# Kernel optimization log

Hardware: AMD Instinct MI355X
Metric: run time of the kernel (lower is better)

Reference implementation:

```python
import jax, jax.numpy as jnp
import numpy as np

B, S, IN, E, H, NL = 64, 512, 1024, 128, 8, 4
D = E // H  # head dim = 16


def setup_inputs() -> dict:
    key = jax.random.key(0)
    ks = jax.random.split(key, 12)
    rn = lambda k, shape: jax.random.normal(k, shape, jnp.float32) * 0.02
    x = jax.random.normal(ks[0], (B, S, IN), jnp.float32)
    # per-recording valid lengths; recording 0 full-length so no attention key row is all-masked
    lengths = jax.random.randint(ks[1], (B,), 1, S + 1).at[0].set(S)
    key_padding_mask = jnp.arange(S)[None, :] >= lengths[:, None]  # (B,S) True = pad
    return {
        'x': x,
        'key_padding_mask': key_padding_mask,
        'embed_w': rn(ks[2], (IN, E)), 'embed_b': jnp.zeros((E,), jnp.float32),
        'qkv_w': rn(ks[3], (NL, 3, E, E)), 'qkv_b': jnp.zeros((NL, 3, E), jnp.float32),
        'out_w': rn(ks[4], (NL, E, E)), 'out_b': jnp.zeros((NL, E), jnp.float32),
        'ln_g': jnp.ones((NL, E), jnp.float32), 'ln_b': jnp.zeros((NL, E), jnp.float32),
        'ff1_w': rn(ks[5], (NL, E, 4 * E)), 'ff1_b': jnp.zeros((NL, 4 * E), jnp.float32),
        'ff2_w': rn(ks[6], (NL, 4 * E, E)), 'ff2_b': jnp.zeros((NL, E), jnp.float32),
        'fc1_w': rn(ks[7], (E, 32)), 'fc1_b': jnp.zeros((32,), jnp.float32),
        'fc2_w': rn(ks[8], (32, 1)), 'fc2_b': jnp.zeros((1,), jnp.float32),
    }


def _ln(x, g, b):
    m = x.mean(-1, keepdims=True)
    v = x.var(-1, keepdims=True)
    return (x - m) / jnp.sqrt(v + 1e-5) * g + b


def _pos_enc(s, e):
    pos = jnp.arange(s, dtype=jnp.float32)[:, None]
    i = jnp.arange(e)[None, :]
    angle = pos / jnp.power(jnp.float32(10000.0), (2 * (i // 2)).astype(jnp.float32) / e)
    return jnp.where(i % 2 == 0, jnp.sin(angle), jnp.cos(angle))  # (S,E)


def reference(x, key_padding_mask, embed_w, embed_b, qkv_w, qkv_b, out_w, out_b,
              ln_g, ln_b, ff1_w, ff1_b, ff2_w, ff2_b, fc1_w, fc1_b, fc2_w, fc2_b):
    h = x @ embed_w + embed_b  # (B,S,E)
    pe = _pos_enc(S, E)
    scale = 1.0 / jnp.sqrt(jnp.float32(D))
    # module uses batch_first=False MHA on (B,S,E): attention runs across recordings.
    # key_padding_mask.T -> (S,B): masked keys are recordings, per epoch position.
    keymask = key_padding_mask.T[:, None, None, :]  # (S,1,1,B)
    for l in range(NL):
        h = h + pe[None]  # pos enc re-added every block (as in source)
        res = h
        q = (h @ qkv_w[l, 0] + qkv_b[l, 0]).reshape(B, S, H, D)
        k = (h @ qkv_w[l, 1] + qkv_b[l, 1]).reshape(B, S, H, D)
        v = (h @ qkv_w[l, 2] + qkv_b[l, 2]).reshape(B, S, H, D)
        scores = jnp.einsum('ishd,jshd->shij', q, k) * scale  # (S,H,B,B)
        scores = jnp.where(keymask, -jnp.inf, scores)
        attn = jax.nn.softmax(scores, axis=-1)
        o = jnp.einsum('shij,jshd->ishd', attn, v).reshape(B, S, E)
        o = o @ out_w[l] + out_b[l]
        h = _ln(o + res, ln_g[l], ln_b[l])
        res = h
        ffo = jax.nn.relu(h @ ff1_w[l] + ff1_b[l]) @ ff2_w[l] + ff2_b[l]
        h = _ln(ffo + res, ln_g[l], ln_b[l])  # same LN params reused, as in source
    # masked mean pool over epochs (vectorized replacement of the python loop)
    valid = (~key_padding_mask).astype(h.dtype)  # (B,S)
    mean = jnp.einsum('bse,bs->be', h, valid) / valid.sum(axis=1)[:, None]
    out = jax.nn.relu(mean @ fc1_w + fc1_b) @ fc2_w + fc2_b  # (B,1)
    return jax.nn.sigmoid(out)
```

## Files before the change

kernel.cpp:

```cpp
#include <hip/hip_runtime.h>

#define Bb 64
#define Ss 512
#define INn 1024
#define Ee 128
#define Hh 8
#define Dd 16
#define NLl 4

typedef unsigned short u16;
typedef __attribute__((ext_vector_type(8))) short short8;
typedef __attribute__((ext_vector_type(4))) float f32x4;

__device__ __forceinline__ float b2f(unsigned u) { return __uint_as_float(u << 16); }
__device__ __forceinline__ u16 f2b(float f) {
    unsigned u = __float_as_uint(f);
    unsigned r = u + 0x7FFFu + ((u >> 16) & 1u);
    return (u16)(r >> 16);
}
__device__ __forceinline__ uint2 pk4(float4 f) {
    uint2 r;
    r.x = (unsigned)f2b(f.x) | ((unsigned)f2b(f.y) << 16);
    r.y = (unsigned)f2b(f.z) | ((unsigned)f2b(f.w) << 16);
    return r;
}

#define GLOAD_LDS16(g, l) __builtin_amdgcn_global_load_lds( \
    (const __attribute__((address_space(1))) void*)(g),     \
    (__attribute__((address_space(3))) void*)(l), 16, 0, 0)

__global__ __launch_bounds__(256) void prep_kernel(const unsigned char* __restrict__ m,
                                                   int* __restrict__ lengths,
                                                   float* __restrict__ pe,
                                                   const float* __restrict__ ew,
                                                   const float* __restrict__ qw,
                                                   const float* __restrict__ ow,
                                                   const float* __restrict__ f1w,
                                                   const float* __restrict__ f2w,
                                                   u16* __restrict__ we, u16* __restrict__ wq,
                                                   u16* __restrict__ wo, u16* __restrict__ wf1,
                                                   u16* __restrict__ wf2) {
    const int bid = blockIdx.x, tid = threadIdx.x;
    if (bid == 0) {
        __shared__ int lf[3];
        __shared__ int part[256];
        if (tid < 3) lf[tid] = 0;
        __syncthreads();
        int l0 = 0, l1 = 0, l23 = 0;
        for (int i = tid * 128; i < tid * 128 + 128; ++i) {
            if (m[i]) { int md = i & 3; if (md == 0) l0 = 1; else if (md == 1) l1 = 1; else l23 = 1; }
        }
        if (l0) atomicOr(&lf[0], 1);
        if (l1) atomicOr(&lf[1], 1);
        if (l23) atomicOr(&lf[2], 1);
        __syncthreads();
        int enc = lf[1] ? 1 : (lf[2] ? 2 : 0);
        int b = tid >> 2, q = tid & 3, cnt = 0;
        for (int s = q * 128; s < q * 128 + 128; ++s) {
            int idx = b * Ss + s;
            int mm;
            if (enc == 1)      mm = (m[idx] != 0);
            else if (enc == 2) mm = (((const float*)(const void*)m)[idx] != 0.0f);
            else               mm = (((const int*)(const void*)m)[idx] != 0);
            cnt += (mm == 0);
        }
        part[tid] = cnt;
        __syncthreads();
        if (tid < 64)
            lengths[tid] = part[tid * 4] + part[tid * 4 + 1] + part[tid * 4 + 2] + part[tid * 4 + 3];
        return;
    }
    if (bid <= 2) {
        for (int i = tid; i < 32768; i += 256) {
            int idx = (bid - 1) * 32768 + i;
            int s = idx >> 7, e = idx & 127;
            float expo = (float)(2 * (e >> 1)) * (1.0f / 128.0f);
            float freq = powf(10000.0f, -expo);
            float angle = (float)s * freq;
            pe[idx] = (e & 1) ? cosf(angle) : sinf(angle);
        }
        return;
    }
    int tb = bid - 3;
    const float* src; u16* dst; int K, N, tile;
    if (tb < 32)       { src = ew;  dst = we;  K = 1024; N = 128; tile = tb; }
    else if (tb < 80)  { int b = tb - 32;  int mat = b >> 2; src = qw  + (size_t)mat * 16384; dst = wq  + (size_t)mat * 16384; K = 128; N = 128; tile = b & 3; }
    else if (tb < 96)  { int b = tb - 80;  int mat = b >> 2; src = ow  + (size_t)mat * 16384; dst = wo  + (size_t)mat * 16384; K = 128; N = 128; tile = b & 3; }
    else if (tb < 160) { int b = tb - 96;  int mat = b >> 4; src = f1w + (size_t)mat * 65536; dst = wf1 + (size_t)mat * 65536; K = 128; N = 512; tile = b & 15; }
    else               { int b = tb - 160; int mat = b >> 4; src = f2w + (size_t)mat * 65536; dst = wf2 + (size_t)mat * 65536; K = 512; N = 128; tile = b & 15; }
    int ktiles = K >> 6;
    int k0 = (tile % ktiles) * 64, n0 = (tile / ktiles) * 64;
    __shared__ __align__(16) u16 t_s[64 * 68];
    int r = tid >> 2, cq = (tid & 3) * 16;
    const float* sp = src + (size_t)(k0 + r) * N + n0 + cq;
#pragma unroll
    for (int i = 0; i < 4; ++i) {
        float4 f = *(const float4*)(sp + 4 * i);
        *(uint2*)&t_s[r * 68 + cq + 4 * i] = pk4(f);
    }
    __syncthreads();
    u16 tmp[16];
#pragma unroll
    for (int kk = 0; kk < 16; ++kk) tmp[kk] = t_s[(cq + kk) * 68 + r];
    int rowg = n0 + r;
    int x = (rowg & 7) << 3;
    u16* base = dst + (size_t)rowg * K;
    *(uint4*)(base + ((k0 + cq) ^ x))     = ((uint4*)tmp)[0];
    *(uint4*)(base + ((k0 + cq + 8) ^ x)) = ((uint4*)tmp)[1];
}

__global__ __launch_bounds__(256) void embed_gemm(const float* __restrict__ X,
                                                  const u16* __restrict__ Wt,
                                                  const float* __restrict__ bias,
                                                  const float* __restrict__ pe,
                                                  u16* __restrict__ C) {
    __shared__ __align__(16) u16 Af[64 * 68];
    __shared__ __align__(16) u16 Bs[128 * 64];
    const int tid = threadIdx.x;
    const int w = tid >> 6, lane = tid & 63, l16 = lane & 15, lhi = lane >> 4;
    const int row0 = blockIdx.x * 64;
    const int xr = (l16 & 7) << 3;
    f32x4 acc[8];
#pragma unroll
    for (int ni = 0; ni < 8; ++ni) acc[ni] = (f32x4){0.f, 0.f, 0.f, 0.f};

    const int ar = tid >> 2, ak = (tid & 3) * 16;
    const int crow = tid >> 3, cc8 = (tid & 7) * 8;
    const int wave_lds = w * 512;
    const u16* Bbase = Wt + cc8;
    const float* Arow = X + (size_t)(row0 + ar) * 1024 + ak;

    for (int k0 = 0; k0 < 1024; k0 += 64) {
        __syncthreads();
#pragma unroll
        for (int i = 0; i < 4; ++i)
            GLOAD_LDS16(Bbase + (size_t)(i * 32 + crow) * 1024 + k0, &Bs[i * 2048 + wave_lds]);
#pragma unroll
        for (int i = 0; i < 4; ++i) {
            float4 f = *(const float4*)(Arow + k0 + 4 * i);
            *(uint2*)&Af[ar * 68 + ak + 4 * i] = pk4(f);
        }
        __syncthreads();
#pragma unroll
        for (int ks = 0; ks < 2; ++ks) {
            short8 af;
            ((uint2*)&af)[0] = *(const uint2*)&Af[(w * 16 + l16) * 68 + ks * 32 + lhi * 8];
            ((uint2*)&af)[1] = *(const uint2*)&Af[(w * 16 + l16) * 68 + ks * 32 + lhi * 8 + 4];
#pragma unroll
            for (int ni = 0; ni < 8; ++ni) {
                short8 bfr = *(const short8*)&Bs[(ni * 16 + l16) * 64 + ((ks * 32 + lhi * 8) ^ xr)];
                acc[ni] = __builtin_amdgcn_mfma_f32_16x16x32_bf16(af, bfr, acc[ni], 0, 0, 0);
            }
        }
    }
    float biasr[8];
#pragma unroll
    for (int ni = 0; ni < 8; ++ni) biasr[ni] = bias[ni * 16 + l16];
#pragma unroll
    for (int reg = 0; reg < 4; ++reg) {
        int r = row0 + w * 16 + lhi * 4 + reg;
        int s = r & 511;
        int bidx = r >> 9;
        int orow = s * 64 + bidx;
        int xo = (bidx & 7) << 3;
        const float* per = pe + (size_t)s * 128;
        u16* crw = C + (size_t)orow * 128;
#pragma unroll
        for (int ni = 0; ni < 8; ++ni) {
            int c = ni * 16 + l16;
            crw[c ^ xo] = f2b(acc[ni][reg] + biasr[ni] + per[c]);
        }
    }
}

__global__ __launch_bounds__(256) void qkv_gemm(const u16* __restrict__ A,
                                                const u16* __restrict__ Wt,
                                                const float* __restrict__ bias,
                                                u16* __restrict__ Cq,
                                                u16* __restrict__ Ckv) {
    __shared__ __align__(16) u16 As[128 * 128];
    __shared__ __align__(16) u16 Bs[128 * 128];
    const int tid = threadIdx.x, w = tid >> 6, lane = tid & 63;
    const int l16 = lane & 15, lhi = lane >> 4;
    const int row0 = blockIdx.x * 128, col0 = blockIdx.y * 128;
    const int so = w * 512 + lane * 8;
    const int xr = (l16 & 7) << 3;
#pragma unroll
    for (int i = 0; i < 8; ++i) {
        GLOAD_LDS16(A + (size_t)row0 * 128 + i * 2048 + so, &As[i * 2048 + w * 512]);
        GLOAD_LDS16(Wt + (size_t)col0 * 128 + i * 2048 + so, &Bs[i * 2048 + w * 512]);
    }
    __syncthreads();
    f32x4 acc[2][8];
#pragma unroll
    for (int mi = 0; mi < 2; ++mi)
#pragma unroll
        for (int ni = 0; ni < 8; ++ni) acc[mi][ni] = (f32x4){0.f, 0.f, 0.f, 0.f};
#pragma unroll
    for (int ks = 0; ks < 4; ++ks) {
        const int ko = (ks * 32 + lhi * 8) ^ xr;
        short8 af[2], bfr[8];
#pragma unroll
        for (int mi = 0; mi < 2; ++mi)
            af[mi] = *(const short8*)&As[(w * 32 + mi * 16 + l16) * 128 + ko];
#pragma unroll
        for (int ni = 0; ni < 8; ++ni)
            bfr[ni] = *(const short8*)&Bs[(ni * 16 + l16) * 128 + ko];
#pragma unroll
        for (int mi = 0; mi < 2; ++mi)
#pragma unroll
            for (int ni = 0; ni < 8; ++ni)
                acc[mi][ni] = __builtin_amdgcn_mfma_f32_16x16x32_bf16(af[mi], bfr[ni], acc[mi][ni], 0, 0, 0);
    }
    float biasr[8];
#pragma unroll
    for (int ni = 0; ni < 8; ++ni) biasr[ni] = bias[col0 + ni * 16 + l16];
#pragma unroll
    for (int mi = 0; mi < 2; ++mi)
#pragma unroll
        for (int reg = 0; reg < 4; ++reg) {
            int r = row0 + w * 32 + mi * 16 + lhi * 4 + reg;
            u16* crw; int cbase;
            if (col0 == 0) { crw = Cq + (size_t)r * 128; cbase = 0; }
            else           { crw = Ckv + (size_t)r * 256; cbase = col0 - 128; }
#pragma unroll
            for (int ni = 0; ni < 8; ++ni)
                crw[cbase + ni * 16 + l16] = f2b(acc[mi][ni][reg] + biasr[ni]);
        }
}

__global__ __launch_bounds__(256) void attnout_kernel(const u16* __restrict__ qb,
                                                      const u16* __restrict__ kvb,
                                                      const u16* __restrict__ wo,
                                                      const float* __restrict__ outb,
                                                      const int* __restrict__ lengths,
                                                      const float* __restrict__ gamma,
                                                      const float* __restrict__ beta,
                                                      u16* __restrict__ h) {
    const int s = blockIdx.x;
    const int tid = threadIdx.x, w = tid >> 6, lane = tid & 63;
    const int l16 = lane & 15, lhi = lane >> 4;
    __shared__ __align__(16) u16 Vt[8 * 16 * 72];
    __shared__ __align__(16) u16 Ps[4 * 64 * 72];
    __shared__ __align__(16) u16 o_s[64 * 136];
    __shared__ int len_s[64];

    {
        int j = tid >> 2, c = tid & 3;
        const u16* src = kvb + ((size_t)(s * 64 + j)) * 256 + 128 + c * 32;
        u16 tmp[32];
        ((uint4*)tmp)[0] = *(const uint4*)src;
        ((uint4*)tmp)[1] = *(const uint4*)(src + 8);
        ((uint4*)tmp)[2] = *(const uint4*)(src + 16);
        ((uint4*)tmp)[3] = *(const uint4*)(src + 24);
#pragma unroll
        for (int e = 0; e < 32; ++e) {
            int hh = 2 * c + (e >> 4), d = e & 15;
            Vt[hh * 1152 + d * 72 + j] = tmp[e];
        }
    }
    if (tid < 64) len_s[tid] = lengths[tid];
    __syncthreads();

    bool mk[4];
#pragma unroll
    for (int jt = 0; jt < 4; ++jt) mk[jt] = (s >= len_s[jt * 16 + l16]);

    u16* pw = Ps + w * 4608;
#pragma unroll
    for (int hp = 0; hp < 2; ++hp) {
        const int hh = w * 2 + hp;
        short8 af[4];
#pragma unroll
        for (int it = 0; it < 4; ++it) {
            af[it] = (short8){0, 0, 0, 0, 0, 0, 0, 0};
            if (lhi < 2)
                af[it] = *(const short8*)(qb + ((size_t)(s * 64 + it * 16 + l16)) * 128 + hh * 16 + lhi * 8);
        }
        f32x4 sf[4][4];
#pragma unroll
        for (int jt = 0; jt < 4; ++jt) {
            short8 bf = (short8){0, 0, 0, 0, 0, 0, 0, 0};
            if (lhi < 2)
                bf = *(const short8*)(kvb + ((size_t)(s * 64 + jt * 16 + l16)) * 256 + hh * 16 + lhi * 8);
#pragma unroll
            for (int it = 0; it < 4; ++it)
                sf[it][jt] = __builtin_amdgcn_mfma_f32_16x16x32_bf16(af[it], bf, (f32x4){0.f, 0.f, 0.f, 0.f}, 0, 0, 0);
        }
        float inv[4][4];
#pragma unroll
        for (int it = 0; it < 4; ++it) {
#pragma unroll
            for (int reg = 0; reg < 4; ++reg) {
                float vv[4], mx = -1e30f;
#pragma unroll
                for (int jt = 0; jt < 4; ++jt) {
                    float xv = mk[jt] ? -1e30f : sf[it][jt][reg] * 0.25f;
                    vv[jt] = xv; mx = fmaxf(mx, xv);
                }
                mx = fmaxf(mx, __shfl_xor(mx, 1)); mx = fmaxf(mx, __shfl_xor(mx, 2));
                mx = fmaxf(mx, __shfl_xor(mx, 4)); mx = fmaxf(mx, __shfl_xor(mx, 8));
                float e4[4], sum = 0.f;
#pragma unroll
                for (int jt = 0; jt < 4; ++jt) {
                    float e = mk[jt] ? 0.f : __expf(vv[jt] - mx);
                    e4[jt] = e; sum += e;
                }
                sum += __shfl_xor(sum, 1); sum += __shfl_xor(sum, 2);
                sum += __shfl_xor(sum, 4); sum += __shfl_xor(sum, 8);
                inv[it][reg] = 1.0f / sum;
                int prow = it * 16 + lhi * 4 + reg;
#pragma unroll
                for (int jt = 0; jt < 4; ++jt)
                    pw[prow * 72 + jt * 16 + l16] = f2b(e4[jt]);
            }
        }
        f32x4 ao[4];
#pragma unroll
        for (int it = 0; it < 4; ++it) ao[it] = (f32x4){0.f, 0.f, 0.f, 0.f};
        short8 vb[2];
#pragma unroll
        for (int ksv = 0; ksv < 2; ++ksv)
            vb[ksv] = *(const short8*)&Vt[hh * 1152 + l16 * 72 + ksv * 32 + lhi * 8];
#pragma unroll
        for (int it = 0; it < 4; ++it)
#pragma unroll
            for (int ksv = 0; ksv < 2; ++ksv) {
                short8 pa = *(const short8*)&pw[(it * 16 + l16) * 72 + ksv * 32 + lhi * 8];
                ao[it] = __builtin_amdgcn_mfma_f32_16x16x32_bf16(pa, vb[ksv], ao[it], 0, 0, 0);
            }
#pragma unroll
        for (int it = 0; it < 4; ++it)
#pragma unroll
            for (int reg = 0; reg < 4; ++reg)
                o_s[(it * 16 + lhi * 4 + reg) * 136 + hh * 16 + l16] = f2b(ao[it][reg] * inv[it][reg]);
    }
    __syncthreads();

    const int xr = (l16 & 7) << 3;
    f32x4 acc[8];
#pragma unroll
    for (int ni = 0; ni < 8; ++ni) acc[ni] = (f32x4){0.f, 0.f, 0.f, 0.f};
#pragma unroll
    for (int ks = 0; ks < 4; ++ks) {
        short8 af = *(const short8*)&o_s[(w * 16 + l16) * 136 + ks * 32 + lhi * 8];
#pragma unroll
        for (int ni = 0; ni < 8; ++ni) {
            short8 bf = *(const short8*)(wo + (size_t)(ni * 16 + l16) * 128 + ((ks * 32 + lhi * 8) ^ xr));
            acc[ni] = __builtin_amdgcn_mfma_f32_16x16x32_bf16(af, bf, acc[ni], 0, 0, 0);
        }
    }
    float biasr[8], gr[8], br[8];
#pragma unroll
    for (int ni = 0; ni < 8; ++ni) {
        int c = ni * 16 + l16;
        biasr[ni] = outb[c]; gr[ni] = gamma[c]; br[ni] = beta[c];
    }
#pragma unroll
    for (int reg = 0; reg < 4; ++reg) {
        int row = w * 16 + lhi * 4 + reg;
        int xo = (row & 7) << 3;
        size_t rbase = ((size_t)(s * 64 + row)) * 128;
        float v[8], sm = 0.f, s2 = 0.f;
#pragma unroll
        for (int ni = 0; ni < 8; ++ni) {
            float x = acc[ni][reg] + biasr[ni] + b2f(h[rbase + ((ni * 16 + l16) ^ xo)]);
            v[ni] = x; sm += x; s2 += x * x;
        }
        sm += __shfl_xor(sm, 1); sm += __shfl_xor(sm, 2);
        sm += __shfl_xor(sm, 4); sm += __shfl_xor(sm, 8);
        s2 += __shfl_xor(s2, 1); s2 += __shfl_xor(s2, 2);
        s2 += __shfl_xor(s2, 4); s2 += __shfl_xor(s2, 8);
        float mean = sm * (1.0f / 128.0f);
        float var = s2 * (1.0f / 128.0f) - mean * mean;
        float rstd = rsqrtf(fmaxf(var, 0.0f) + 1e-5f);
#pragma unroll
        for (int ni = 0; ni < 8; ++ni)
            h[rbase + ((ni * 16 + l16) ^ xo)] = f2b((v[ni] - mean) * rstd * gr[ni] + br[ni]);
    }
}

__global__ __launch_bounds__(256) void ff_fused(const u16* __restrict__ hbuf,
                                                const u16* __restrict__ w1t,
                                                const u16* __restrict__ w2t,
                                                const float* __restrict__ b1,
                                                const float* __restrict__ b2,
                                                const float* __restrict__ gamma,
                                                const float* __restrict__ beta,
                                                const float* __restrict__ pe,
                                                u16* __restrict__ hout) {
    __shared__ __align__(16) u16 A_s[16384];
    __shared__ __align__(16) u16 W1_s[16384];
    __shared__ __align__(16) u16 W2_s[16384];
    __shared__ __align__(16) u16 T_s[16384];
    const int tid = threadIdx.x, w = tid >> 6, lane = tid & 63;
    const int l16 = lane & 15, lhi = lane >> 4;
    const int row0 = blockIdx.x * 128;
    const int so = w * 512 + lane * 8;
    const int xr = (l16 & 7) << 3;
#pragma unroll
    for (int i = 0; i < 8; ++i)
        GLOAD_LDS16(hbuf + (size_t)row0 * 128 + i * 2048 + so, &A_s[i * 2048 + w * 512]);

    f32x4 acc2[2][8];
#pragma unroll
    for (int mi = 0; mi < 2; ++mi)
#pragma unroll
        for (int ni = 0; ni < 8; ++ni) acc2[mi][ni] = (f32x4){0.f, 0.f, 0.f, 0.f};

    for (int nc = 0; nc < 4; ++nc) {
        __syncthreads();
#pragma unroll
        for (int i = 0; i < 8; ++i) {
            GLOAD_LDS16(w1t + nc * 16384 + i * 2048 + so, &W1_s[i * 2048 + w * 512]);
            int slot = i * 2048 + so;
            GLOAD_LDS16(w2t + (size_t)(slot >> 7) * 512 + nc * 128 + (slot & 127),
                        &W2_s[i * 2048 + w * 512]);
        }
        __syncthreads();
        f32x4 acc1[2][8];
#pragma unroll
        for (int mi = 0; mi < 2; ++mi)
#pragma unroll
            for (int ni = 0; ni < 8; ++ni) acc1[mi][ni] = (f32x4){0.f, 0.f, 0.f, 0.f};
#pragma unroll
        for (int ks = 0; ks < 4; ++ks) {
            const int ko = (ks * 32 + lhi * 8) ^ xr;
            short8 af[2], bfr[8];
#pragma unroll
            for (int mi = 0; mi < 2; ++mi)
                af[mi] = *(const short8*)&A_s[(w * 32 + mi * 16 + l16) * 128 + ko];
#pragma unroll
            for (int ni = 0; ni < 8; ++ni)
                bfr[ni] = *(const short8*)&W1_s[(ni * 16 + l16) * 128 + ko];
#pragma unroll
            for (int mi = 0; mi < 2; ++mi)
#pragma unroll
                for (int ni = 0; ni < 8; ++ni)
                    acc1[mi][ni] = __builtin_amdgcn_mfma_f32_16x16x32_bf16(af[mi], bfr[ni], acc1[mi][ni], 0, 0, 0);
        }
        float bb[8];
#pragma unroll
        for (int ni = 0; ni < 8; ++ni) bb[ni] = b1[nc * 128 + ni * 16 + l16];
#pragma unroll
        for (int mi = 0; mi < 2; ++mi)
#pragma unroll
            for (int reg = 0; reg < 4; ++reg) {
                int xt = ((lhi * 4 + reg) & 7) << 3;
#pragma unroll
                for (int ni = 0; ni < 8; ++ni)
                    T_s[(w * 32 + mi * 16 + lhi * 4 + reg) * 128 + ((ni * 16 + l16) ^ xt)] =
                        f2b(fmaxf(acc1[mi][ni][reg] + bb[ni], 0.0f));
            }
#pragma unroll
        for (int ks = 0; ks < 4; ++ks) {
            const int ko = (ks * 32 + lhi * 8) ^ xr;
            short8 pa[2], bfr[8];
#pragma unroll
            for (int mi = 0; mi < 2; ++mi)
                pa[mi] = *(const short8*)&T_s[(w * 32 + mi * 16 + l16) * 128 + ko];
#pragma unroll
            for (int ni = 0; ni < 8; ++ni)
                bfr[ni] = *(const short8*)&W2_s[(ni * 16 + l16) * 128 + ko];
#pragma unroll
            for (int mi = 0; mi < 2; ++mi)
#pragma unroll
                for (int ni = 0; ni < 8; ++ni)
                    acc2[mi][ni] = __builtin_amdgcn_mfma_f32_16x16x32_bf16(pa[mi], bfr[ni], acc2[mi][ni], 0, 0, 0);
        }
    }
    float b2r[8], gr[8], br[8];
#pragma unroll
    for (int ni = 0; ni < 8; ++ni) {
        int c = ni * 16 + l16;
        b2r[ni] = b2[c]; gr[ni] = gamma[c]; br[ni] = beta[c];
    }
#pragma unroll
    for (int mi = 0; mi < 2; ++mi)
#pragma unroll
        for (int reg = 0; reg < 4; ++reg) {
            int lrow = w * 32 + mi * 16 + lhi * 4 + reg;
            int r = row0 + lrow;
            int xo = (lrow & 7) << 3;
            float v[8], sm = 0.f, s2 = 0.f;
#pragma unroll
            for (int ni = 0; ni < 8; ++ni) {
                float x = acc2[mi][ni][reg] + b2r[ni] + b2f(A_s[lrow * 128 + ((ni * 16 + l16) ^ xo)]);
                v[ni] = x; sm += x; s2 += x * x;
            }
            sm += __shfl_xor(sm, 1); sm += __shfl_xor(sm, 2);
            sm += __shfl_xor(sm, 4); sm += __shfl_xor(sm, 8);
            s2 += __shfl_xor(s2, 1); s2 += __shfl_xor(s2, 2);
            s2 += __shfl_xor(s2, 4); s2 += __shfl_xor(s2, 8);
            float mean = sm * (1.0f / 128.0f);
            float var = s2 * (1.0f / 128.0f) - mean * mean;
            float rstd = rsqrtf(fmaxf(var, 0.0f) + 1e-5f);
            u16* crw = hout + (size_t)r * 128;
#pragma unroll
            for (int ni = 0; ni < 8; ++ni) {
                int c = ni * 16 + l16;
                float val = (v[ni] - mean) * rstd * gr[ni] + br[ni];
                if (pe) val += pe[(size_t)(r >> 6) * 128 + c];
                crw[c ^ xo] = f2b(val);
            }
        }
}

__global__ __launch_bounds__(256) void poolhead_kernel(const u16* __restrict__ h,
                                                       const int* __restrict__ lengths,
                                                       const float* __restrict__ fc1w,
                                                       const float* __restrict__ fc1b,
                                                       const float* __restrict__ fc2w,
                                                       const float* __restrict__ fc2b,
                                                       float* __restrict__ out) {
    int b = blockIdx.x, tid = threadIdx.x;
    int e = tid & 127, half = tid >> 7;
    int len = lengths[b];
    int ep = e ^ ((b & 7) << 3);
    float s = 0.0f;
    for (int t = half; t < len; t += 2) s += b2f(h[((size_t)(t * 64 + b)) * 128 + ep]);
    __shared__ float red[256];
    __shared__ float mp[128];
    __shared__ float z[32];
    red[tid] = s;
    __syncthreads();
    if (tid < 128) mp[tid] = (red[tid] + red[tid + 128]) / (float)len;
    __syncthreads();
    if (tid < 32) {
        float a = fc1b[tid];
        for (int k = 0; k < 128; ++k) a = fmaf(mp[k], fc1w[k * 32 + tid], a);
        z[tid] = fmaxf(a, 0.0f);
    }
    __syncthreads();
    if (tid == 0) {
        float a = fc2b[0];
#pragma unroll
        for (int t = 0; t < 32; ++t) a = fmaf(z[t], fc2w[t], a);
        out[b] = 1.0f / (1.0f + expf(-a));
    }
}

extern "C" void kernel_launch(void* const* d_in, const int* in_sizes, int n_in,
                              void* d_out, int out_size, void* d_ws, size_t ws_size,
                              hipStream_t stream) {
    (void)in_sizes; (void)n_in; (void)out_size; (void)ws_size;
    const float* x        = (const float*)d_in[0];
    const unsigned char* mask = (const unsigned char*)d_in[1];
    const float* embed_w  = (const float*)d_in[2];
    const float* embed_b  = (const float*)d_in[3];
    const float* qkv_w    = (const float*)d_in[4];
    const float* qkv_b    = (const float*)d_in[5];
    const float* out_w    = (const float*)d_in[6];
    const float* out_b    = (const float*)d_in[7];
    const float* ln_g     = (const float*)d_in[8];
    const float* ln_b     = (const float*)d_in[9];
    const float* ff1_w    = (const float*)d_in[10];
    const float* ff1_b    = (const float*)d_in[11];
    const float* ff2_w    = (const float*)d_in[12];
    const float* ff2_b    = (const float*)d_in[13];
    const float* fc1_w    = (const float*)d_in[14];
    const float* fc1_b    = (const float*)d_in[15];
    const float* fc2_w    = (const float*)d_in[16];
    const float* fc2_b    = (const float*)d_in[17];

    char* wsb = (char*)d_ws;
    int*   lengths = (int*)wsb;
    float* pe      = (float*)(wsb + 512);
    u16* wt_embed  = (u16*)(wsb + 262656);
    u16* wt_qkv    = (u16*)(wsb + 524800);
    u16* wt_out    = (u16*)(wsb + 918016);
    u16* wt_ff1    = (u16*)(wsb + 1049088);
    u16* wt_ff2    = (u16*)(wsb + 1573376);
    u16* hbuf      = (u16*)(wsb + 2097664);
    u16* qb        = (u16*)(wsb + 10486272);
    u16* kvb       = (u16*)(wsb + 18874880);

    prep_kernel<<<227, 256, 0, stream>>>(mask, lengths, pe,
                                         embed_w, qkv_w, out_w, ff1_w, ff2_w,
                                         wt_embed, wt_qkv, wt_out, wt_ff1, wt_ff2);

    embed_gemm<<<512, 256, 0, stream>>>(x, wt_embed, embed_b, pe, hbuf);

    for (int l = 0; l < NLl; ++l) {
        qkv_gemm<<<dim3(256, 3), 256, 0, stream>>>(
            hbuf, wt_qkv + (size_t)l * 49152, qkv_b + l * 384, qb, kvb);
        attnout_kernel<<<512, 256, 0, stream>>>(
            qb, kvb, wt_out + (size_t)l * 16384, out_b + l * 128,
            lengths, ln_g + l * 128, ln_b + l * 128, hbuf);
        ff_fused<<<256, 256, 0, stream>>>(
            hbuf, wt_ff1 + (size_t)l * 65536, wt_ff2 + (size_t)l * 65536,
            ff1_b + l * 512, ff2_b + l * 128,
            ln_g + l * 128, ln_b + l * 128, (l < 3) ? pe : nullptr, hbuf);
    }

    poolhead_kernel<<<64, 256, 0, stream>>>(hbuf, lengths, fc1_w, fc1_b, fc2_w, fc2_b,
                                            (float*)d_out);
}
```

Baseline: 427.7 us.

## Fuse next-layer QKV projection into FF kernel and double-buffer weight loads

Folds the next layer's QKV projection into the tail of ff_fused: the LN output tile is kept in shared memory and multiplied by the next layer's QKV weights loaded into the freed LDS arena. This removes three separate qkv_gemm launches and their re-read of hbuf. The FF weight loads are restructured so the next W1/W2 chunks are prefetched while the current chunk computes, and embed_gemm double-buffers its B tile. In exchange, ff_fused uses a 128KB LDS arena, which limits occupancy, and each block does more work in its epilogue.

```diff
diff --git a/kernel.cpp b/kernel.cpp
--- a/kernel.cpp
+++ b/kernel.cpp
@@ -115,7 +115,7 @@
                                                   const float* __restrict__ pe,
                                                   u16* __restrict__ C) {
     __shared__ __align__(16) u16 Af[64 * 68];
-    __shared__ __align__(16) u16 Bs[128 * 64];
+    __shared__ __align__(16) u16 Bs[2][128 * 64];
     const int tid = threadIdx.x;
     const int w = tid >> 6, lane = tid & 63, l16 = lane & 15, lhi = lane >> 4;
     const int row0 = blockIdx.x * 64;
@@ -130,17 +130,25 @@
     const u16* Bbase = Wt + cc8;
     const float* Arow = X + (size_t)(row0 + ar) * 1024 + ak;
 
-    for (int k0 = 0; k0 < 1024; k0 += 64) {
+#pragma unroll
+    for (int i = 0; i < 4; ++i)
+        GLOAD_LDS16(Bbase + (size_t)(i * 32 + crow) * 1024, &Bs[0][i * 2048 + wave_lds]);
+
+    for (int it = 0; it < 16; ++it) {
+        const int k0 = it * 64;
         __syncthreads();
-#pragma unroll
-        for (int i = 0; i < 4; ++i)
-            GLOAD_LDS16(Bbase + (size_t)(i * 32 + crow) * 1024 + k0, &Bs[i * 2048 + wave_lds]);
 #pragma unroll
         for (int i = 0; i < 4; ++i) {
             float4 f = *(const float4*)(Arow + k0 + 4 * i);
             *(uint2*)&Af[ar * 68 + ak + 4 * i] = pk4(f);
         }
         __syncthreads();
+        if (it < 15) {
+#pragma unroll
+            for (int i = 0; i < 4; ++i)
+                GLOAD_LDS16(Bbase + (size_t)(i * 32 + crow) * 1024 + k0 + 64,
+                            &Bs[(it + 1) & 1][i * 2048 + wave_lds]);
+        }
 #pragma unroll
         for (int ks = 0; ks < 2; ++ks) {
             short8 af;
@@ -148,7 +156,7 @@
             ((uint2*)&af)[1] = *(const uint2*)&Af[(w * 16 + l16) * 68 + ks * 32 + lhi * 8 + 4];
 #pragma unroll
             for (int ni = 0; ni < 8; ++ni) {
-                short8 bfr = *(const short8*)&Bs[(ni * 16 + l16) * 64 + ((ks * 32 + lhi * 8) ^ xr)];
+                short8 bfr = *(const short8*)&Bs[it & 1][(ni * 16 + l16) * 64 + ((ks * 32 + lhi * 8) ^ xr)];
                 acc[ni] = __builtin_amdgcn_mfma_f32_16x16x32_bf16(af, bfr, acc[ni], 0, 0, 0);
             }
         }
@@ -388,19 +396,33 @@
                                                 const float* __restrict__ gamma,
                                                 const float* __restrict__ beta,
                                                 const float* __restrict__ pe,
-                                                u16* __restrict__ hout) {
-    __shared__ __align__(16) u16 A_s[16384];
-    __shared__ __align__(16) u16 W1_s[16384];
-    __shared__ __align__(16) u16 W2_s[16384];
-    __shared__ __align__(16) u16 T_s[16384];
+                                                u16* __restrict__ hout,
+                                                const u16* __restrict__ wqn,
+                                                const float* __restrict__ qbn,
+                                                u16* __restrict__ Cq,
+                                                u16* __restrict__ Ckv) {
+    __shared__ __align__(16) u16 arena[65536];
+    u16* A_s  = arena;
+    u16* W1_s = arena + 16384;
+    u16* W2_s = arena + 32768;
+    u16* T_s  = arena + 49152;
+    u16* Wq_s = arena + 16384;
     const int tid = threadIdx.x, w = tid >> 6, lane = tid & 63;
     const int l16 = lane & 15, lhi = lane >> 4;
     const int row0 = blockIdx.x * 128;
     const int so = w * 512 + lane * 8;
     const int xr = (l16 & 7) << 3;
+
 #pragma unroll
     for (int i = 0; i < 8; ++i)
         GLOAD_LDS16(hbuf + (size_t)row0 * 128 + i * 2048 + so, &A_s[i * 2048 + w * 512]);
+#pragma unroll
+    for (int i = 0; i < 8; ++i) {
+        GLOAD_LDS16(w1t + i * 2048 + so, &W1_s[i * 2048 + w * 512]);
+        int slot = i * 2048 + so;
+        GLOAD_LDS16(w2t + (size_t)(slot >> 7) * 512 + (slot & 127), &W2_s[i * 2048 + w * 512]);
+    }
+    __syncthreads();
 
     f32x4 acc2[2][8];
 #pragma unroll
@@ -409,15 +431,6 @@
         for (int ni = 0; ni < 8; ++ni) acc2[mi][ni] = (f32x4){0.f, 0.f, 0.f, 0.f};
 
     for (int nc = 0; nc < 4; ++nc) {
-        __syncthreads();
-#pragma unroll
-        for (int i = 0; i < 8; ++i) {
-            GLOAD_LDS16(w1t + nc * 16384 + i * 2048 + so, &W1_s[i * 2048 + w * 512]);
-            int slot = i * 2048 + so;
-            GLOAD_LDS16(w2t + (size_t)(slot >> 7) * 512 + nc * 128 + (slot & 127),
-                        &W2_s[i * 2048 + w * 512]);
-        }
-        __syncthreads();
         f32x4 acc1[2][8];
 #pragma unroll
         for (int mi = 0; mi < 2; ++mi)
@@ -452,6 +465,12 @@
                     T_s[(w * 32 + mi * 16 + lhi * 4 + reg) * 128 + ((ni * 16 + l16) ^ xt)] =
                         f2b(fmaxf(acc1[mi][ni][reg] + bb[ni], 0.0f));
             }
+        __syncthreads();
+        if (nc < 3) {
+#pragma unroll
+            for (int i = 0; i < 8; ++i)
+                GLOAD_LDS16(w1t + (nc + 1) * 16384 + i * 2048 + so, &W1_s[i * 2048 + w * 512]);
+        }
 #pragma unroll
         for (int ks = 0; ks < 4; ++ks) {
             const int ko = (ks * 32 + lhi * 8) ^ xr;
@@ -468,6 +487,20 @@
                 for (int ni = 0; ni < 8; ++ni)
                     acc2[mi][ni] = __builtin_amdgcn_mfma_f32_16x16x32_bf16(pa[mi], bfr[ni], acc2[mi][ni], 0, 0, 0);
         }
+        __syncthreads();
+        if (nc < 3) {
+#pragma unroll
+            for (int i = 0; i < 8; ++i) {
+                int slot = i * 2048 + so;
+                GLOAD_LDS16(w2t + (size_t)(slot >> 7) * 512 + (nc + 1) * 128 + (slot & 127),
+                            &W2_s[i * 2048 + w * 512]);
+            }
+        }
+    }
+    if (wqn) {
+#pragma unroll
+        for (int i = 0; i < 24; ++i)
+            GLOAD_LDS16(wqn + i * 2048 + so, &Wq_s[i * 2048 + w * 512]);
     }
     float b2r[8], gr[8], br[8];
 #pragma unroll
@@ -501,9 +534,52 @@
                 int c = ni * 16 + l16;
                 float val = (v[ni] - mean) * rstd * gr[ni] + br[ni];
                 if (pe) val += pe[(size_t)(r >> 6) * 128 + c];
-                crw[c ^ xo] = f2b(val);
-            }
-        }
+                u16 hv = f2b(val);
+                crw[c ^ xo] = hv;
+                if (wqn) A_s[lrow * 128 + (c ^ xo)] = hv;
+            }
+        }
+    if (!wqn) return;
+
+    __syncthreads();
+    for (int cc = 0; cc < 3; ++cc) {
+        f32x4 acc[2][8];
+#pragma unroll
+        for (int mi = 0; mi < 2; ++mi)
+#pragma unroll
+            for (int ni = 0; ni < 8; ++ni) acc[mi][ni] = (f32x4){0.f, 0.f, 0.f, 0.f};
+#pragma unroll
+        for (int ks = 0; ks < 4; ++ks) {
+            const int ko = (ks * 32 + lhi * 8) ^ xr;
+            short8 af[2], bfr[8];
+#pragma unroll
+            for (int mi = 0; mi < 2; ++mi)
+                af[mi] = *(const short8*)&A_s[(w * 32 + mi * 16 + l16) * 128 + ko];
+#pragma unroll
+            for (int ni = 0; ni < 8; ++ni)
+                bfr[ni] = *(const short8*)&Wq_s[(cc * 128 + ni * 16 + l16) * 128 + ko];
+#pragma unroll
+            for (int mi = 0; mi < 2; ++mi)
+#pragma unroll
+                for (int ni = 0; ni < 8; ++ni)
+                    acc[mi][ni] = __builtin_amdgcn_mfma_f32_16x16x32_bf16(af[mi], bfr[ni], acc[mi][ni], 0, 0, 0);
+        }
+        float biasr[8];
+#pragma unroll
+        for (int ni = 0; ni < 8; ++ni) biasr[ni] = qbn[cc * 128 + ni * 16 + l16];
+#pragma unroll
+        for (int mi = 0; mi < 2; ++mi)
+#pragma unroll
+            for (int reg = 0; reg < 4; ++reg) {
+                int r = row0 + w * 32 + mi * 16 + lhi * 4 + reg;
+                u16* crw; int cbase;
+                if (cc == 0) { crw = Cq + (size_t)r * 128; cbase = 0; }
+                else         { crw = Ckv + (size_t)r * 256; cbase = (cc - 1) * 128; }
+#pragma unroll
+                for (int ni = 0; ni < 8; ++ni)
+                    crw[cbase + ni * 16 + l16] = f2b(acc[mi][ni][reg] + biasr[ni]);
+            }
+    }
 }
 
 __global__ __launch_bounds__(256) void poolhead_kernel(const u16* __restrict__ h,
@@ -581,16 +657,21 @@
 
     embed_gemm<<<512, 256, 0, stream>>>(x, wt_embed, embed_b, pe, hbuf);
 
+    qkv_gemm<<<dim3(256, 3), 256, 0, stream>>>(
+        hbuf, wt_qkv, qkv_b, qb, kvb);
+
     for (int l = 0; l < NLl; ++l) {
-        qkv_gemm<<<dim3(256, 3), 256, 0, stream>>>(
-            hbuf, wt_qkv + (size_t)l * 49152, qkv_b + l * 384, qb, kvb);
         attnout_kernel<<<512, 256, 0, stream>>>(
             qb, kvb, wt_out + (size_t)l * 16384, out_b + l * 128,
             lengths, ln_g + l * 128, ln_b + l * 128, hbuf);
+        bool mergeq = (l < 3);
         ff_fused<<<256, 256, 0, stream>>>(
             hbuf, wt_ff1 + (size_t)l * 65536, wt_ff2 + (size_t)l * 65536,
             ff1_b + l * 512, ff2_b + l * 128,
-            ln_g + l * 128, ln_b + l * 128, (l < 3) ? pe : nullptr, hbuf);
+            ln_g + l * 128, ln_b + l * 128, (l < 3) ? pe : nullptr, hbuf,
+            mergeq ? wt_qkv + (size_t)(l + 1) * 49152 : nullptr,
+            mergeq ? qkv_b + (l + 1) * 384 : nullptr,
+            qb, kvb);
     }
 
     poolhead_kernel<<<64, 256, 0, stream>>>(hbuf, lengths, fc1_w, fc1_b, fc2_w, fc2_b,
```

New measurement: 427.8 us. No clear change (+0.0%).
